# Optimization experiments

Measured on AMD Instinct MI355X. Metric: run time of the kernel, lower is better.

Reference implementation:

```python
import jax, jax.numpy as jnp
import numpy as np

# ---- static config (mirrors ConvCapsules init + assumed ConvCaps1 input) ----
KERNEL, STRIDE = 3, 2
CHILD_SPACE, CHILD_CAPS = 14, 32
PARENT_CAPS, ROUTINGS = 32, 3
BATCH = 8
FINAL_LAMBDA = 0.01
EPS = 1e-9
PARENT_SPACE = (CHILD_SPACE - KERNEL) // STRIDE + 1  # 6
P2 = PARENT_SPACE ** 2   # 36
KK = KERNEL ** 2         # 9
C2 = CHILD_SPACE ** 2    # 196


def _child_index_map():
    # For each parent spatial position p and kernel offset k (row-major, as
    # produced by kernel_tile's depthwise-conv trick), the flat child spatial
    # index. Also counts how many parents each child spatial position feeds.
    idx = np.zeros((P2, KK), dtype=np.int32)
    cnt = np.zeros((C2,), dtype=np.float32)
    for r in range(PARENT_SPACE):
        for c in range(PARENT_SPACE):
            p = r * PARENT_SPACE + c
            for i in range(KERNEL):
                for j in range(KERNEL):
                    s = (r * STRIDE + i) * CHILD_SPACE + (c * STRIDE + j)
                    idx[p, i * KERNEL + j] = s
                    cnt[s] += 1.0
    return idx, cnt

CHILD_IDX, PARENTS_PER_CHILD = _child_index_map()


def setup_inputs() -> dict:
    key = jax.random.key(0)
    k1, k2, k3, k4 = jax.random.split(key, 4)
    # last dim 17 = 16 pose + 1 activation; activation must be >= 0
    inputs = jax.random.uniform(k1, (BATCH, CHILD_SPACE, CHILD_SPACE, CHILD_CAPS, 17), dtype=jnp.float32)
    w = jax.random.normal(k2, (KK * CHILD_CAPS, PARENT_CAPS, 4, 4), dtype=jnp.float32)
    beta_v = jax.random.normal(k3, (1, 1, 1, PARENT_CAPS, 1), dtype=jnp.float32)
    beta_a = jax.random.normal(k4, (1, 1, 1, PARENT_CAPS, 1), dtype=jnp.float32)
    return {"inputs": inputs, "w": w, "beta_v": beta_v, "beta_a": beta_a}


def _kernel_tile(x):
    # x: [N,H,W,caps,A] -> [N, ps, ps, kk, caps, A]  (im2col gather)
    row = (np.arange(PARENT_SPACE) * STRIDE)[:, None] + np.arange(KERNEL)[None, :]  # (ps,k)
    x = x[:, row]             # [N, ps, k, W, caps, A]
    x = x[:, :, :, row]       # [N, ps, k, ps, k, caps, A]
    x = jnp.transpose(x, (0, 1, 3, 2, 4, 5, 6))  # [N, ps, ps, k, k, caps, A]
    return x.reshape(x.shape[0], PARENT_SPACE, PARENT_SPACE, KK, x.shape[-2], x.shape[-1])


def _em_routing(votes, act_i, beta_v, beta_a):
    # votes: [N, P2, KK*ci, o, 16]; act_i: [N, P2, KK*ci, 1, 1]
    N = votes.shape[0]
    ci, o = CHILD_CAPS, PARENT_CAPS
    flat_idx = CHILD_IDX.reshape(-1)  # (P2*KK,)

    # rr init: uniform over all parents (spatial x caps) each child routes to
    ppc = PARENTS_PER_CHILD[CHILD_IDX]  # (P2, KK)
    rr = jnp.asarray((1.0 / (ppc * o)).astype(np.float32))[None, :, :, None, None]
    rr = jnp.broadcast_to(rr, (1, P2, KK, ci, o)).reshape(1, P2, KK * ci, o, 1)

    for it in range(ROUTINGS):
        inv_temp = FINAL_LAMBDA * (1.0 - 0.95 ** (it + 1))
        # ---------------- M-step ----------------
        rr_prime = rr * act_i                                   # [N,P2,KK*ci,o,1]
        rr_sum = jnp.sum(rr_prime, axis=2, keepdims=True)       # [N,P2,1,o,1]
        mean = jnp.sum(rr_prime * votes, axis=2, keepdims=True) / (rr_sum + EPS)  # [N,P2,1,o,16]
        var = jnp.sum(rr_prime * (votes - mean) ** 2, axis=2, keepdims=True) / (rr_sum + EPS) + EPS
        cost_h = (beta_v + 0.5 * jnp.log(var)) * rr_sum          # [N,P2,1,o,16]
        cost = jnp.sum(cost_h, axis=-1, keepdims=True)           # [N,P2,1,o,1]
        cost_mean = jnp.mean(cost, axis=3, keepdims=True)
        cost_stdv = jnp.sqrt(jnp.sum((cost - cost_mean) ** 2, axis=3, keepdims=True) / o)
        act_j = jax.nn.sigmoid(inv_temp * (beta_a + (cost_mean - cost) / (cost_stdv + EPS)))
        if it < ROUTINGS - 1:
            # ---------------- E-step ----------------
            ln_p = (-0.5 * jnp.sum(jnp.log(2.0 * jnp.pi * var), axis=-1, keepdims=True)
                    - jnp.sum((votes - mean) ** 2 / (2.0 * var), axis=-1, keepdims=True))  # [N,P2,KK*ci,o,1]
            zz = jnp.log(act_j + EPS) + ln_p
            zz5 = zz.reshape(N, P2, KK, ci, o)
            # stable softmax over ALL parents (spatial positions x parent caps)
            # of each child, done sparsely via scatter-max / scatter-add keyed
            # on child spatial index
            zmax = jnp.max(zz5, axis=-1).reshape(N, P2 * KK, ci)
            cmax = jnp.full((N, C2, ci), -1e30, zz5.dtype).at[:, flat_idx, :].max(zmax)
            cmax = jax.lax.stop_gradient(cmax)
            e = jnp.exp(zz5 - cmax[:, CHILD_IDX][..., None])     # [N,P2,KK,ci,o]
            denom = jnp.zeros((N, C2, ci), zz5.dtype).at[:, flat_idx, :].add(
                jnp.sum(e, axis=-1).reshape(N, P2 * KK, ci))
            rr = (e / (denom[:, CHILD_IDX][..., None] + EPS)).reshape(N, P2, KK * ci, o, 1)

    pose_out = mean.reshape(N, PARENT_SPACE, PARENT_SPACE, o, 16)
    act_out = act_j.reshape(N, PARENT_SPACE, PARENT_SPACE, o, 1)
    return pose_out, act_out


def reference(inputs, w, beta_v, beta_a):
    N = inputs.shape[0]
    pose = inputs[..., :16]
    act = inputs[..., 16:]
    pose_t = _kernel_tile(pose)  # [N,ps,ps,KK,ci,16]
    act_t = _kernel_tile(act)    # [N,ps,ps,KK,ci,1]
    pose_u = pose_t.reshape(N * P2, KK * CHILD_CAPS, 4, 4)
    act_u = act_t.reshape(N, P2, KK * CHILD_CAPS, 1, 1)
    # votes: each child's 4x4 pose times learned 4x4 transform per parent cap
    votes = jnp.einsum('nkab,kobc->nkoac', pose_u, w)  # [N*P2, KK*ci, o, 4, 4]
    votes = votes.reshape(N, P2, KK * CHILD_CAPS, PARENT_CAPS, 16)
    pose_out, act_out = _em_routing(votes, act_u, beta_v, beta_a)
    return jnp.concatenate([act_out, pose_out], axis=-1)  # [N,ps,ps,o,17]
```

## Files before the change

### kernel.cpp

```cpp
#include <hip/hip_runtime.h>
#include <math.h>

#define PS 6
#define P2 36
#define CI 32
#define OO 32
#define KC 288
#define KCO 9216
#define EPSF 1e-9f
#define LOG2PI_F 1.8378770664093455f

#define ZZ_OFF   0u
#define RR_OFF   2654208u
#define WT_OFF   5308416u
#define PART_OFF 5455872u

__device__ __forceinline__ int covr(int x){
  int cnt = 0;
#pragma unroll
  for (int r = 0; r < 6; ++r) { int i = x - 2*r; cnt += (i >= 0 && i <= 2) ? 1 : 0; }
  return cnt;
}

__global__ __launch_bounds__(256) void wtrans_kernel(const float* __restrict__ w,
                                                     float* __restrict__ wT)
{
  int e = blockIdx.x * 256 + threadIdx.x;
  int b = e & 3, o = (e >> 2) & 31, c = (e >> 7) & 3, k = e >> 9;
  wT[e] = w[k*512 + o*16 + b*4 + c];
}

template<bool FIRST>
__global__ __launch_bounds__(256, 5) void moments_kernel(
    const float* __restrict__ inp, const float* __restrict__ wT,
    const float* __restrict__ rrg, float* __restrict__ part)
{
  __shared__ float s_pose[72*16];
  __shared__ float s_ra[72];
  __shared__ float s_red[4*1056];

  const int blk = blockIdx.x;
  const int np = blk >> 2, k4 = blk & 3;
  const int n = np / P2, p = np % P2;
  const int pr = p / PS, pc = p % PS;
  const int t = threadIdx.x;
  const int k0 = k4 * 72;

  const float* ibase = inp + (size_t)n * (196*32*17);
  for (int e = t; e < 72*16; e += 256) {
    int kl = e >> 4, h = e & 15;
    int k = k0 + kl;
    int kk = k >> 5, ci = k & 31;
    s_pose[e] = ibase[(((pr*2 + kk/3)*14 + (pc*2 + kk%3))*32 + ci)*17 + h];
  }
  if (FIRST && t < 72) {
    int k = k0 + t; int kk = k >> 5, ci = k & 31;
    int x = pr*2 + kk/3, y = pc*2 + kk%3;
    float a = ibase[((x*14 + y)*32 + ci)*17 + 16];
    s_ra[t] = a / (float)(covr(x) * covr(y) * OO);
  }
  __syncthreads();

  const int q = t >> 5, o = t & 31;
  float srr = 0.f;
  float m1[16], m2[16];
#pragma unroll
  for (int j = 0; j < 16; ++j) { m1[j] = 0.f; m2[j] = 0.f; }

  const float* rp = rrg + (size_t)np * KCO;
#pragma unroll 3
  for (int ks = 0; ks < 9; ++ks) {
    int kl = q*9 + ks;
    int k  = k0 + kl;
    float rra = FIRST ? s_ra[kl] : rp[(k << 5) + o];
    const float4* pk  = (const float4*)s_pose + (kl << 2);
    const float4* wkb = (const float4*)wT + ((size_t)k << 7) + o;
    float4 w0 = wkb[0], w1 = wkb[32], w2 = wkb[64], w3 = wkb[96];
    srr += rra;
#pragma unroll
    for (int a = 0; a < 4; ++a) {
      float4 P = pk[a];
      float v0 = P.x*w0.x + P.y*w0.y + P.z*w0.z + P.w*w0.w;
      float v1 = P.x*w1.x + P.y*w1.y + P.z*w1.z + P.w*w1.w;
      float v2 = P.x*w2.x + P.y*w2.y + P.z*w2.z + P.w*w2.w;
      float v3 = P.x*w3.x + P.y*w3.y + P.z*w3.z + P.w*w3.w;
      float r0 = rra*v0, r1 = rra*v1, r2 = rra*v2, r3 = rra*v3;
      m1[a*4+0] += r0;    m1[a*4+1] += r1;    m1[a*4+2] += r2;    m1[a*4+3] += r3;
      m2[a*4+0] += r0*v0; m2[a*4+1] += r1*v1; m2[a*4+2] += r2*v2; m2[a*4+3] += r3*v3;
    }
  }

  srr += __shfl_xor(srr, 32, 64);
#pragma unroll
  for (int j = 0; j < 16; ++j) {
    m1[j] += __shfl_xor(m1[j], 32, 64);
    m2[j] += __shfl_xor(m2[j], 32, 64);
  }
  {
    const int lane = t & 63, wv = t >> 6;
    if (lane < 32) {
      float* rb = s_red + wv*1056 + lane*33;
      rb[0] = srr;
#pragma unroll
      for (int j = 0; j < 16; ++j) { rb[1+j] = m1[j]; rb[17+j] = m2[j]; }
    }
  }
  __syncthreads();
  float* pb = part + (size_t)blk * 1056;
  for (int u = t; u < 1056; u += 256) {
    float s = s_red[u] + s_red[1056+u] + s_red[2112+u] + s_red[3168+u];
    pb[u] = s;
  }
}

template<int IT>
__global__ __launch_bounds__(512, 4) void zzstats_kernel(
    const float* __restrict__ inp, const float* __restrict__ wT,
    const float* __restrict__ part,
    const float* __restrict__ beta_v, const float* __restrict__ beta_a,
    float* __restrict__ zzg)
{
  __shared__ float s_pose[72*16];
  __shared__ float s_mean[512];
  __shared__ float s_i2v[512];
  __shared__ float s_cost[OO];
  __shared__ float s_lvs[OO];
  __shared__ float s_lc[OO];

  const int blk = blockIdx.x;
  const int np = blk >> 2, k4 = blk & 3;
  const int n = np / P2, p = np % P2;
  const int pr = p / PS, pc = p % PS;
  const int t = threadIdx.x;
  const int k0 = k4 * 72;

  const float* ibase = inp + (size_t)n * (196*32*17);
  for (int e = t; e < 72*16; e += 512) {
    int kl = e >> 4, h = e & 15;
    int k = k0 + kl;
    int kk = k >> 5, ci = k & 31;
    s_pose[e] = ibase[(((pr*2 + kk/3)*14 + (pc*2 + kk%3))*32 + ci)*17 + h];
  }

  {
    const int so = t >> 4, h = t & 15;
    const float* pb = part + (size_t)np * 4224 + so*33;
    float rs = pb[0]        + pb[1056]        + pb[2112]        + pb[3168];
    float a1 = pb[1+h]      + pb[1056+1+h]    + pb[2112+1+h]    + pb[3168+1+h];
    float a2 = pb[17+h]     + pb[1056+17+h]   + pb[2112+17+h]   + pb[3168+17+h];
    float S    = rs + EPSF;
    float mean = a1 / S;
    float var  = fmaxf(a2 / S - mean*mean, 0.f) + EPSF;
    float lvh  = __logf(var);
    float ch   = (beta_v[so] + 0.5f * lvh) * rs;
    float lv   = lvh;
#pragma unroll
    for (int d = 1; d < 16; d <<= 1) {
      ch += __shfl_xor(ch, d, 64);
      lv += __shfl_xor(lv, d, 64);
    }
    s_mean[t] = mean;
    s_i2v[t]  = 0.5f / var;
    if (h == 0) { s_cost[so] = ch; s_lvs[so] = lv; }
  }
  __syncthreads();

  if (t < OO) {
    float cm = 0.f;
#pragma unroll
    for (int oi = 0; oi < OO; ++oi) cm += s_cost[oi];
    cm *= (1.f / OO);
    float ssq = 0.f;
#pragma unroll
    for (int oi = 0; oi < OO; ++oi) { float d = s_cost[oi] - cm; ssq += d*d; }
    float sd = sqrtf(ssq * (1.f / OO));
    const float INVT = (IT==0) ? 5.0e-4f : 9.75e-4f;
    float arg = INVT * (beta_a[t] + (cm - s_cost[t]) / (sd + EPSF));
    float aj  = 1.f / (1.f + __expf(-arg));
    s_lc[t] = __logf(aj + EPSF) - 0.5f * (s_lvs[t] + 16.f * LOG2PI_F);
  }
  __syncthreads();

  {
    const int oz = t & 31;
    const float lc = s_lc[oz];
    const float4* mo4 = (const float4*)(s_mean + (oz << 4));
    const float4* io4 = (const float4*)(s_i2v  + (oz << 4));
    float4 M0 = mo4[0], M1 = mo4[1], M2 = mo4[2], M3 = mo4[3];
    float4 I0 = io4[0], I1 = io4[1], I2 = io4[2], I3 = io4[3];
    float* zb = zzg + (size_t)np * KCO + ((size_t)k0 << 5);
    for (int r = t; r < 2304; r += 512) {
      int kl = r >> 5;
      int k  = k0 + kl;
      const float4* pk  = (const float4*)s_pose + (kl << 2);
      const float4* wkb = (const float4*)wT + ((size_t)k << 7) + oz;
      float4 w0 = wkb[0], w1 = wkb[32], w2 = wkb[64], w3 = wkb[96];
      float ssum = 0.f;
      float4 P;
      P = pk[0];
      {
        float x0 = P.x*w0.x + P.y*w0.y + P.z*w0.z + P.w*w0.w;
        float x1 = P.x*w1.x + P.y*w1.y + P.z*w1.z + P.w*w1.w;
        float x2 = P.x*w2.x + P.y*w2.y + P.z*w2.z + P.w*w2.w;
        float x3 = P.x*w3.x + P.y*w3.y + P.z*w3.z + P.w*w3.w;
        float d0 = x0-M0.x, d1 = x1-M0.y, d2 = x2-M0.z, d3 = x3-M0.w;
        ssum += d0*d0*I0.x + d1*d1*I0.y + d2*d2*I0.z + d3*d3*I0.w;
      }
      P = pk[1];
      {
        float x0 = P.x*w0.x + P.y*w0.y + P.z*w0.z + P.w*w0.w;
        float x1 = P.x*w1.x + P.y*w1.y + P.z*w1.z + P.w*w1.w;
        float x2 = P.x*w2.x + P.y*w2.y + P.z*w2.z + P.w*w2.w;
        float x3 = P.x*w3.x + P.y*w3.y + P.z*w3.z + P.w*w3.w;
        float d0 = x0-M1.x, d1 = x1-M1.y, d2 = x2-M1.z, d3 = x3-M1.w;
        ssum += d0*d0*I1.x + d1*d1*I1.y + d2*d2*I1.z + d3*d3*I1.w;
      }
      P = pk[2];
      {
        float x0 = P.x*w0.x + P.y*w0.y + P.z*w0.z + P.w*w0.w;
        float x1 = P.x*w1.x + P.y*w1.y + P.z*w1.z + P.w*w1.w;
        float x2 = P.x*w2.x + P.y*w2.y + P.z*w2.z + P.w*w2.w;
        float x3 = P.x*w3.x + P.y*w3.y + P.z*w3.z + P.w*w3.w;
        float d0 = x0-M2.x, d1 = x1-M2.y, d2 = x2-M2.z, d3 = x3-M2.w;
        ssum += d0*d0*I2.x + d1*d1*I2.y + d2*d2*I2.z + d3*d3*I2.w;
      }
      P = pk[3];
      {
        float x0 = P.x*w0.x + P.y*w0.y + P.z*w0.z + P.w*w0.w;
        float x1 = P.x*w1.x + P.y*w1.y + P.z*w1.z + P.w*w1.w;
        float x2 = P.x*w2.x + P.y*w2.y + P.z*w2.z + P.w*w2.w;
        float x3 = P.x*w3.x + P.y*w3.y + P.z*w3.z + P.w*w3.w;
        float d0 = x0-M3.x, d1 = x1-M3.y, d2 = x2-M3.z, d3 = x3-M3.w;
        ssum += d0*d0*I3.x + d1*d1*I3.y + d2*d2*I3.z + d3*d3*I3.w;
      }
      zb[r] = lc - ssum;
    }
  }
}

__global__ __launch_bounds__(512) void statsout_kernel(
    const float* __restrict__ part,
    const float* __restrict__ beta_v, const float* __restrict__ beta_a,
    float* __restrict__ out)
{
  __shared__ float s_cost[OO];
  const int np = blockIdx.x;
  const int t = threadIdx.x;
  const int o = t >> 4, h = t & 15;

  const float* pb = part + (size_t)np * 4224 + o*33;
  float rs = pb[0]    + pb[1056]      + pb[2112]      + pb[3168];
  float a1 = pb[1+h]  + pb[1056+1+h]  + pb[2112+1+h]  + pb[3168+1+h];
  float a2 = pb[17+h] + pb[1056+17+h] + pb[2112+17+h] + pb[3168+17+h];
  float S = rs + EPSF;
  float mean = a1 / S;
  float var  = fmaxf(a2 / S - mean*mean, 0.f) + EPSF;
  float ch   = (beta_v[o] + 0.5f * __logf(var)) * rs;
#pragma unroll
  for (int d = 1; d < 16; d <<= 1) ch += __shfl_xor(ch, d, 64);
  if (h == 0) s_cost[o] = ch;
  __syncthreads();

  float cm = 0.f;
#pragma unroll
  for (int oi = 0; oi < OO; ++oi) cm += s_cost[oi];
  cm *= (1.f / OO);
  float ssq = 0.f;
#pragma unroll
  for (int oi = 0; oi < OO; ++oi) { float d = s_cost[oi] - cm; ssq += d*d; }
  float sd = sqrtf(ssq * (1.f / OO));
  float arg = 1.42625e-3f * (beta_a[o] + (cm - s_cost[o]) / (sd + EPSF));
  float aj  = 1.f / (1.f + __expf(-arg));

  out[((size_t)np*OO + o)*17 + 1 + h] = mean;
  if (h == 0) out[((size_t)np*OO + o)*17] = aj;
}

__global__ __launch_bounds__(256) void childnorm_kernel(
    const float* __restrict__ inp, const float* __restrict__ zzg,
    float* __restrict__ rrg)
{
  const int tg = blockIdx.x * 256 + threadIdx.x;
  const int g = tg >> 2, slot = tg & 3;
  const int n   = g / (169*32);
  const int rem = g % (169*32);
  const int sc  = rem >> 5, ci = rem & 31;
  const int x = sc / 13, y = sc % 13;

  int base = -1; int cnt = 0;
#pragma unroll
  for (int r = 0; r < 6; ++r) {
    int i = x - 2*r;
    if (i < 0 || i > 2) continue;
#pragma unroll
    for (int c2 = 0; c2 < 6; ++c2) {
      int j = y - 2*c2;
      if (j < 0 || j > 2) continue;
      if (cnt == slot) base = (((n*P2 + r*6+c2)*9 + i*3+j)*CI + ci) << 5;
      ++cnt;
    }
  }

  const float4* z4 = (base >= 0) ? (const float4*)(zzg + base) : (const float4*)zzg;
  float4 zv[8];
#pragma unroll
  for (int q = 0; q < 8; ++q) zv[q] = z4[q];

  float m = -1e30f;
  if (base >= 0) {
#pragma unroll
    for (int q = 0; q < 8; ++q) {
      float4 v = zv[q];
      m = fmaxf(m, fmaxf(fmaxf(v.x, v.y), fmaxf(v.z, v.w)));
    }
  }
  m = fmaxf(m, __shfl_xor(m, 1, 64));
  m = fmaxf(m, __shfl_xor(m, 2, 64));

  float den = 0.f;
  float e[32];
  if (base >= 0) {
#pragma unroll
    for (int q = 0; q < 8; ++q) {
      float4 v = zv[q];
      e[q*4+0] = __expf(v.x - m); e[q*4+1] = __expf(v.y - m);
      e[q*4+2] = __expf(v.z - m); e[q*4+3] = __expf(v.w - m);
      den += e[q*4+0] + e[q*4+1] + e[q*4+2] + e[q*4+3];
    }
  }
  den += __shfl_xor(den, 1, 64);
  den += __shfl_xor(den, 2, 64);

  const float act = inp[(((size_t)n*196 + x*14 + y)*32 + ci)*17 + 16];
  float s = act / (den + EPSF);

  if (base >= 0) {
    float4* r4 = (float4*)(rrg + base);
#pragma unroll
    for (int q = 0; q < 8; ++q) {
      float4 rv;
      rv.x = e[q*4+0]*s; rv.y = e[q*4+1]*s; rv.z = e[q*4+2]*s; rv.w = e[q*4+3]*s;
      r4[q] = rv;
    }
  }
}

extern "C" void kernel_launch(void* const* d_in, const int* in_sizes, int n_in,
                              void* d_out, int out_size, void* d_ws, size_t ws_size,
                              hipStream_t stream)
{
  (void)in_sizes; (void)n_in; (void)out_size; (void)ws_size;
  const float* inp = (const float*)d_in[0];
  const float* w   = (const float*)d_in[1];
  const float* bv  = (const float*)d_in[2];
  const float* ba  = (const float*)d_in[3];
  float* out = (float*)d_out;
  float* ws  = (float*)d_ws;
  float* zz   = ws + ZZ_OFF;
  float* rr   = ws + RR_OFF;
  float* wT   = ws + WT_OFF;
  float* part = ws + PART_OFF;

  wtrans_kernel<<<576, 256, 0, stream>>>(w, wT);

  moments_kernel<true ><<<1152, 256, 0, stream>>>(inp, wT, rr, part);
  zzstats_kernel<0><<<1152, 512, 0, stream>>>(inp, wT, part, bv, ba, zz);
  childnorm_kernel<<<676, 256, 0, stream>>>(inp, zz, rr);

  moments_kernel<false><<<1152, 256, 0, stream>>>(inp, wT, rr, part);
  zzstats_kernel<1><<<1152, 512, 0, stream>>>(inp, wT, part, bv, ba, zz);
  childnorm_kernel<<<676, 256, 0, stream>>>(inp, zz, rr);

  moments_kernel<false><<<1152, 256, 0, stream>>>(inp, wT, rr, part);
  statsout_kernel<<<288, 512, 0, stream>>>(part, bv, ba, out);
}
```

Measured before the change: 112.4 us.

## Store per-child softmax max/scale instead of full rr tensor; recompute rr in moments

childnorm now writes only a per-child (max, act/denominator) pair instead of the full 9216-per-position routing tensor, and moments_kernel recomputes each routing weight as exp(zz - max) * scale directly from zz. This removes one full-size tensor write and read per routing iteration, in exchange for an extra exp per element inside moments. The moments and zzstats inner loops also gain software prefetching of the next weight and pose values, and moments' occupancy hint drops from 5 to 4.

```diff
diff --git a/kernel.cpp b/kernel.cpp
--- a/kernel.cpp
+++ b/kernel.cpp
@@ -11,9 +11,9 @@
 #define LOG2PI_F 1.8378770664093455f
 
 #define ZZ_OFF   0u
-#define RR_OFF   2654208u
-#define WT_OFF   5308416u
-#define PART_OFF 5455872u
+#define WT_OFF   2654208u
+#define PART_OFF 2801664u
+#define MS_OFF   4018176u
 
 __device__ __forceinline__ int covr(int x){
   int cnt = 0;
@@ -31,12 +31,14 @@
 }
 
 template<bool FIRST>
-__global__ __launch_bounds__(256, 5) void moments_kernel(
+__global__ __launch_bounds__(256, 4) void moments_kernel(
     const float* __restrict__ inp, const float* __restrict__ wT,
-    const float* __restrict__ rrg, float* __restrict__ part)
+    const float* __restrict__ zzg, const float2* __restrict__ msg,
+    float* __restrict__ part)
 {
   __shared__ float s_pose[72*16];
-  __shared__ float s_ra[72];
+  __shared__ float s_m[72];
+  __shared__ float s_s[72];
   __shared__ float s_red[4*1056];
 
   const int blk = blockIdx.x;
@@ -53,11 +55,17 @@
     int kk = k >> 5, ci = k & 31;
     s_pose[e] = ibase[(((pr*2 + kk/3)*14 + (pc*2 + kk%3))*32 + ci)*17 + h];
   }
-  if (FIRST && t < 72) {
+  if (t < 72) {
     int k = k0 + t; int kk = k >> 5, ci = k & 31;
     int x = pr*2 + kk/3, y = pc*2 + kk%3;
-    float a = ibase[((x*14 + y)*32 + ci)*17 + 16];
-    s_ra[t] = a / (float)(covr(x) * covr(y) * OO);
+    if (FIRST) {
+      float a = ibase[((x*14 + y)*32 + ci)*17 + 16];
+      s_m[t] = a / (float)(covr(x) * covr(y) * OO);
+    } else {
+      float2 ms = msg[((size_t)(n*169 + x*13 + y))*32 + ci];
+      s_m[t] = ms.x;
+      s_s[t] = ms.y;
+    }
   }
   __syncthreads();
 
@@ -67,26 +75,68 @@
 #pragma unroll
   for (int j = 0; j < 16; ++j) { m1[j] = 0.f; m2[j] = 0.f; }
 
-  const float* rp = rrg + (size_t)np * KCO;
-#pragma unroll 3
+  const float* zp = zzg + (size_t)np * KCO + ((size_t)k0 << 5) + o;
+
+  float4 A0n, A1n, A2n, A3n, w0n, w1n, w2n, w3n;
+  float zn = 0.f;
+  {
+    int kl = q*9;
+    const float4* pk  = (const float4*)s_pose + (kl << 2);
+    A0n = pk[0]; A1n = pk[1]; A2n = pk[2]; A3n = pk[3];
+    const float4* wkb = (const float4*)wT + ((size_t)(k0 + kl) << 7) + o;
+    w0n = wkb[0]; w1n = wkb[32]; w2n = wkb[64]; w3n = wkb[96];
+    if (!FIRST) zn = zp[kl << 5];
+  }
+#pragma unroll
   for (int ks = 0; ks < 9; ++ks) {
-    int kl = q*9 + ks;
-    int k  = k0 + kl;
-    float rra = FIRST ? s_ra[kl] : rp[(k << 5) + o];
-    const float4* pk  = (const float4*)s_pose + (kl << 2);
-    const float4* wkb = (const float4*)wT + ((size_t)k << 7) + o;
-    float4 w0 = wkb[0], w1 = wkb[32], w2 = wkb[64], w3 = wkb[96];
+    const int kl = q*9 + ks;
+    float4 A0 = A0n, A1 = A1n, A2 = A2n, A3 = A3n;
+    float4 w0 = w0n, w1 = w1n, w2 = w2n, w3 = w3n;
+    float z = zn;
+    if (ks < 8) {
+      const float4* pk  = (const float4*)s_pose + ((kl+1) << 2);
+      A0n = pk[0]; A1n = pk[1]; A2n = pk[2]; A3n = pk[3];
+      const float4* wkb = (const float4*)wT + ((size_t)(k0 + kl + 1) << 7) + o;
+      w0n = wkb[0]; w1n = wkb[32]; w2n = wkb[64]; w3n = wkb[96];
+      if (!FIRST) zn = zp[(kl+1) << 5];
+    }
+    float rra = FIRST ? s_m[kl] : __expf(z - s_m[kl]) * s_s[kl];
     srr += rra;
-#pragma unroll
-    for (int a = 0; a < 4; ++a) {
-      float4 P = pk[a];
-      float v0 = P.x*w0.x + P.y*w0.y + P.z*w0.z + P.w*w0.w;
-      float v1 = P.x*w1.x + P.y*w1.y + P.z*w1.z + P.w*w1.w;
-      float v2 = P.x*w2.x + P.y*w2.y + P.z*w2.z + P.w*w2.w;
-      float v3 = P.x*w3.x + P.y*w3.y + P.z*w3.z + P.w*w3.w;
-      float r0 = rra*v0, r1 = rra*v1, r2 = rra*v2, r3 = rra*v3;
-      m1[a*4+0] += r0;    m1[a*4+1] += r1;    m1[a*4+2] += r2;    m1[a*4+3] += r3;
-      m2[a*4+0] += r0*v0; m2[a*4+1] += r1*v1; m2[a*4+2] += r2*v2; m2[a*4+3] += r3*v3;
+    {
+      float v0 = A0.x*w0.x + A0.y*w0.y + A0.z*w0.z + A0.w*w0.w;
+      float v1 = A0.x*w1.x + A0.y*w1.y + A0.z*w1.z + A0.w*w1.w;
+      float v2 = A0.x*w2.x + A0.y*w2.y + A0.z*w2.z + A0.w*w2.w;
+      float v3 = A0.x*w3.x + A0.y*w3.y + A0.z*w3.z + A0.w*w3.w;
+      float r0=rra*v0, r1=rra*v1, r2=rra*v2, r3=rra*v3;
+      m1[0]+=r0; m1[1]+=r1; m1[2]+=r2; m1[3]+=r3;
+      m2[0]+=r0*v0; m2[1]+=r1*v1; m2[2]+=r2*v2; m2[3]+=r3*v3;
+    }
+    {
+      float v0 = A1.x*w0.x + A1.y*w0.y + A1.z*w0.z + A1.w*w0.w;
+      float v1 = A1.x*w1.x + A1.y*w1.y + A1.z*w1.z + A1.w*w1.w;
+      float v2 = A1.x*w2.x + A1.y*w2.y + A1.z*w2.z + A1.w*w2.w;
+      float v3 = A1.x*w3.x + A1.y*w3.y + A1.z*w3.z + A1.w*w3.w;
+      float r0=rra*v0, r1=rra*v1, r2=rra*v2, r3=rra*v3;
+      m1[4]+=r0; m1[5]+=r1; m1[6]+=r2; m1[7]+=r3;
+      m2[4]+=r0*v0; m2[5]+=r1*v1; m2[6]+=r2*v2; m2[7]+=r3*v3;
+    }
+    {
+      float v0 = A2.x*w0.x + A2.y*w0.y + A2.z*w0.z + A2.w*w0.w;
+      float v1 = A2.x*w1.x + A2.y*w1.y + A2.z*w1.z + A2.w*w1.w;
+      float v2 = A2.x*w2.x + A2.y*w2.y + A2.z*w2.z + A2.w*w2.w;
+      float v3 = A2.x*w3.x + A2.y*w3.y + A2.z*w3.z + A2.w*w3.w;
+      float r0=rra*v0, r1=rra*v1, r2=rra*v2, r3=rra*v3;
+      m1[8]+=r0; m1[9]+=r1; m1[10]+=r2; m1[11]+=r3;
+      m2[8]+=r0*v0; m2[9]+=r1*v1; m2[10]+=r2*v2; m2[11]+=r3*v3;
+    }
+    {
+      float v0 = A3.x*w0.x + A3.y*w0.y + A3.z*w0.z + A3.w*w0.w;
+      float v1 = A3.x*w1.x + A3.y*w1.y + A3.z*w1.z + A3.w*w1.w;
+      float v2 = A3.x*w2.x + A3.y*w2.y + A3.z*w2.z + A3.w*w2.w;
+      float v3 = A3.x*w3.x + A3.y*w3.y + A3.z*w3.z + A3.w*w3.w;
+      float r0=rra*v0, r1=rra*v1, r2=rra*v2, r3=rra*v3;
+      m1[12]+=r0; m1[13]+=r1; m1[14]+=r2; m1[15]+=r3;
+      m2[12]+=r0*v0; m2[13]+=r1*v1; m2[14]+=r2*v2; m2[15]+=r3*v3;
     }
   }
 
@@ -108,8 +158,7 @@
   __syncthreads();
   float* pb = part + (size_t)blk * 1056;
   for (int u = t; u < 1056; u += 256) {
-    float s = s_red[u] + s_red[1056+u] + s_red[2112+u] + s_red[3168+u];
-    pb[u] = s;
+    pb[u] = s_red[u] + s_red[1056+u] + s_red[2112+u] + s_red[3168+u];
   }
 }
 
@@ -145,9 +194,9 @@
   {
     const int so = t >> 4, h = t & 15;
     const float* pb = part + (size_t)np * 4224 + so*33;
-    float rs = pb[0]        + pb[1056]        + pb[2112]        + pb[3168];
-    float a1 = pb[1+h]      + pb[1056+1+h]    + pb[2112+1+h]    + pb[3168+1+h];
-    float a2 = pb[17+h]     + pb[1056+17+h]   + pb[2112+17+h]   + pb[3168+17+h];
+    float rs = pb[0]    + pb[1056]      + pb[2112]      + pb[3168];
+    float a1 = pb[1+h]  + pb[1056+1+h]  + pb[2112+1+h]  + pb[3168+1+h];
+    float a2 = pb[17+h] + pb[1056+17+h] + pb[2112+17+h] + pb[3168+17+h];
     float S    = rs + EPSF;
     float mean = a1 / S;
     float var  = fmaxf(a2 / S - mean*mean, 0.f) + EPSF;
@@ -183,57 +232,69 @@
 
   {
     const int oz = t & 31;
+    const int tq = t >> 5;
     const float lc = s_lc[oz];
     const float4* mo4 = (const float4*)(s_mean + (oz << 4));
     const float4* io4 = (const float4*)(s_i2v  + (oz << 4));
     float4 M0 = mo4[0], M1 = mo4[1], M2 = mo4[2], M3 = mo4[3];
     float4 I0 = io4[0], I1 = io4[1], I2 = io4[2], I3 = io4[3];
     float* zb = zzg + (size_t)np * KCO + ((size_t)k0 << 5);
-    for (int r = t; r < 2304; r += 512) {
-      int kl = r >> 5;
-      int k  = k0 + kl;
-      const float4* pk  = (const float4*)s_pose + (kl << 2);
-      const float4* wkb = (const float4*)wT + ((size_t)k << 7) + oz;
-      float4 w0 = wkb[0], w1 = wkb[32], w2 = wkb[64], w3 = wkb[96];
+
+    float4 w0n, w1n, w2n, w3n;
+    {
+      const float4* wkb = (const float4*)wT + ((size_t)(k0 + tq) << 7) + oz;
+      w0n = wkb[0]; w1n = wkb[32]; w2n = wkb[64]; w3n = wkb[96];
+    }
+#pragma unroll
+    for (int i = 0; i < 5; ++i) {
+      if (i == 4 && tq >= 8) break;
+      const int kl = (i < 4) ? (i*16 + tq) : (64 + tq);
+      float4 w0 = w0n, w1 = w1n, w2 = w2n, w3 = w3n;
+      if (i < 4) {
+        int kln = (i < 3) ? (kl + 16) : (64 + (tq & 7));
+        const float4* wkb = (const float4*)wT + ((size_t)(k0 + kln) << 7) + oz;
+        w0n = wkb[0]; w1n = wkb[32]; w2n = wkb[64]; w3n = wkb[96];
+      }
+      const float4* pk = (const float4*)s_pose + (kl << 2);
       float ssum = 0.f;
-      float4 P;
-      P = pk[0];
+      float4 A;
+      A = pk[0];
       {
-        float x0 = P.x*w0.x + P.y*w0.y + P.z*w0.z + P.w*w0.w;
-        float x1 = P.x*w1.x + P.y*w1.y + P.z*w1.z + P.w*w1.w;
-        float x2 = P.x*w2.x + P.y*w2.y + P.z*w2.z + P.w*w2.w;
-        float x3 = P.x*w3.x + P.y*w3.y + P.z*w3.z + P.w*w3.w;
+        float x0 = A.x*w0.x + A.y*w0.y + A.z*w0.z + A.w*w0.w;
+        float x1 = A.x*w1.x + A.y*w1.y + A.z*w1.z + A.w*w1.w;
+        float x2 = A.x*w2.x + A.y*w2.y + A.z*w2.z + A.w*w2.w;
+        float x3 = A.x*w3.x + A.y*w3.y + A.z*w3.z + A.w*w3.w;
         float d0 = x0-M0.x, d1 = x1-M0.y, d2 = x2-M0.z, d3 = x3-M0.w;
         ssum += d0*d0*I0.x + d1*d1*I0.y + d2*d2*I0.z + d3*d3*I0.w;
       }
-      P = pk[1];
+      A = pk[1];
       {
-        float x0 = P.x*w0.x + P.y*w0.y + P.z*w0.z + P.w*w0.w;
-        float x1 = P.x*w1.x + P.y*w1.y + P.z*w1.z + P.w*w1.w;
-        float x2 = P.x*w2.x + P.y*w2.y + P.z*w2.z + P.w*w2.w;
-        float x3 = P.x*w3.x + P.y*w3.y + P.z*w3.z + P.w*w3.w;
+        float x0 = A.x*w0.x + A.y*w0.y + A.z*w0.z + A.w*w0.w;
+        float x1 = A.x*w1.x + A.y*w1.y + A.z*w1.z + A.w*w1.w;
+        float x2 = A.x*w2.x + A.y*w2.y + A.z*w2.z + A.w*w2.w;
+        float x3 = A.x*w3.x + A.y*w3.y + A.z*w3.z + A.w*w3.w;
         float d0 = x0-M1.x, d1 = x1-M1.y, d2 = x2-M1.z, d3 = x3-M1.w;
         ssum += d0*d0*I1.x + d1*d1*I1.y + d2*d2*I1.z + d3*d3*I1.w;
       }
-      P = pk[2];
+      A = pk[2];
       {
-        float x0 = P.x*w0.x + P.y*w0.y + P.z*w0.z + P.w*w0.w;
-        float x1 = P.x*w1.x + P.y*w1.y + P.z*w1.z + P.w*w1.w;
-        float x2 = P.x*w2.x + P.y*w2.y + P.z*w2.z + P.w*w2.w;
-        float x3 = P.x*w3.x + P.y*w3.y + P.z*w3.z + P.w*w3.w;
+        float x0 = A.x*w0.x + A.y*w0.y + A.z*w0.z + A.w*w0.w;
+        float x1 = A.x*w1.x + A.y*w1.y + A.z*w1.z + A.w*w1.w;
+        float x2 = A.x*w2.x + A.y*w2.y + A.z*w2.z + A.w*w2.w;
+        float x3 = A.x*w3.x + A.y*w3.y + A.z*w3.z + A.w*w3.w;
         float d0 = x0-M2.x, d1 = x1-M2.y, d2 = x2-M2.z, d3 = x3-M2.w;
         ssum += d0*d0*I2.x + d1*d1*I2.y + d2*d2*I2.z + d3*d3*I2.w;
       }
-      P = pk[3];
+      A = pk[3];
       {
-        float x0 = P.x*w0.x + P.y*w0.y + P.z*w0.z + P.w*w0.w;
-        float x1 = P.x*w1.x + P.y*w1.y + P.z*w1.z + P.w*w1.w;
-        float x2 = P.x*w2.x + P.y*w2.y + P.z*w2.z + P.w*w2.w;
-        float x3 = P.x*w3.x + P.y*w3.y + P.z*w3.z + P.w*w3.w;
+        float x0 = A.x*w0.x + A.y*w0.y + A.z*w0.z + A.w*w0.w;
+        float x1 = A.x*w1.x + A.y*w1.y + A.z*w1.z + A.w*w1.w;
+        float x2 = A.x*w2.x + A.y*w2.y + A.z*w2.z + A.w*w2.w;
+        float x3 = A.x*w3.x + A.y*w3.y + A.z*w3.z + A.w*w3.w;
         float d0 = x0-M3.x, d1 = x1-M3.y, d2 = x2-M3.z, d3 = x3-M3.w;
         ssum += d0*d0*I3.x + d1*d1*I3.y + d2*d2*I3.z + d3*d3*I3.w;
       }
-      zb[r] = lc - ssum;
+      zb[(kl << 5) + oz] = lc - ssum;
     }
   }
 }
@@ -278,7 +339,7 @@
 
 __global__ __launch_bounds__(256) void childnorm_kernel(
     const float* __restrict__ inp, const float* __restrict__ zzg,
-    float* __restrict__ rrg)
+    float2* __restrict__ msg)
 {
   const int tg = blockIdx.x * 256 + threadIdx.x;
   const int g = tg >> 2, slot = tg & 3;
@@ -318,30 +379,20 @@
   m = fmaxf(m, __shfl_xor(m, 2, 64));
 
   float den = 0.f;
-  float e[32];
   if (base >= 0) {
 #pragma unroll
     for (int q = 0; q < 8; ++q) {
       float4 v = zv[q];
-      e[q*4+0] = __expf(v.x - m); e[q*4+1] = __expf(v.y - m);
-      e[q*4+2] = __expf(v.z - m); e[q*4+3] = __expf(v.w - m);
-      den += e[q*4+0] + e[q*4+1] + e[q*4+2] + e[q*4+3];
+      den += __expf(v.x-m) + __expf(v.y-m) + __expf(v.z-m) + __expf(v.w-m);
     }
   }
   den += __shfl_xor(den, 1, 64);
   den += __shfl_xor(den, 2, 64);
 
-  const float act = inp[(((size_t)n*196 + x*14 + y)*32 + ci)*17 + 16];
-  float s = act / (den + EPSF);
-
-  if (base >= 0) {
-    float4* r4 = (float4*)(rrg + base);
-#pragma unroll
-    for (int q = 0; q < 8; ++q) {
-      float4 rv;
-      rv.x = e[q*4+0]*s; rv.y = e[q*4+1]*s; rv.z = e[q*4+2]*s; rv.w = e[q*4+3]*s;
-      r4[q] = rv;
-    }
+  if (slot == 0) {
+    const float act = inp[(((size_t)n*196 + x*14 + y)*32 + ci)*17 + 16];
+    float2 ms; ms.x = m; ms.y = act / (den + EPSF);
+    msg[g] = ms;
   }
 }
 
@@ -357,20 +408,20 @@
   float* out = (float*)d_out;
   float* ws  = (float*)d_ws;
   float* zz   = ws + ZZ_OFF;
-  float* rr   = ws + RR_OFF;
   float* wT   = ws + WT_OFF;
   float* part = ws + PART_OFF;
+  float2* msg = (float2*)(ws + MS_OFF);
 
   wtrans_kernel<<<576, 256, 0, stream>>>(w, wT);
 
-  moments_kernel<true ><<<1152, 256, 0, stream>>>(inp, wT, rr, part);
+  moments_kernel<true ><<<1152, 256, 0, stream>>>(inp, wT, zz, msg, part);
   zzstats_kernel<0><<<1152, 512, 0, stream>>>(inp, wT, part, bv, ba, zz);
-  childnorm_kernel<<<676, 256, 0, stream>>>(inp, zz, rr);
-
-  moments_kernel<false><<<1152, 256, 0, stream>>>(inp, wT, rr, part);
+  childnorm_kernel<<<676, 256, 0, stream>>>(inp, zz, msg);
+
+  moments_kernel<false><<<1152, 256, 0, stream>>>(inp, wT, zz, msg, part);
   zzstats_kernel<1><<<1152, 512, 0, stream>>>(inp, wT, part, bv, ba, zz);
-  childnorm_kernel<<<676, 256, 0, stream>>>(inp, zz, rr);
-
-  moments_kernel<false><<<1152, 256, 0, stream>>>(inp, wT, rr, part);
+  childnorm_kernel<<<676, 256, 0, stream>>>(inp, zz, msg);
+
+  moments_kernel<false><<<1152, 256, 0, stream>>>(inp, wT, zz, msg, part);
   statsout_kernel<<<288, 512, 0, stream>>>(part, bv, ba, out);
 }
```

Result: slower. 229.7 us (+104.4%).
